# Kernel tuning notes

Hardware: AMD Instinct MI355X
Metric: run time of the kernel (lower is better)

Reference implementation:

```python
import jax, jax.numpy as jnp
import numpy as np

N_NODES = 100000
N_EDGES = 1600000
D_IN, D_H, D_OUT = 128, 128, 64


def gcn_conv(x, src, dst, W, b, n_nodes):
    """PyG GCNConv (eval): x' = D^{-1/2} (A+I) D^{-1/2} X W + b.
    src/dst already include self-loops."""
    h = x @ W  # [N, d_out] -- transform first (fewer FLOPs when d_out <= d_in)
    deg = jax.ops.segment_sum(jnp.ones_like(dst, dtype=h.dtype), dst, num_segments=n_nodes)
    dinv = jnp.where(deg > 0, jax.lax.rsqrt(deg), 0.0)
    norm = dinv[src] * dinv[dst]  # [E]
    msg = h[src] * norm[:, None]  # gather + scale
    out = jax.ops.segment_sum(msg, dst, num_segments=n_nodes)  # scatter-add
    return out + b


def setup_inputs() -> dict:
    key = jax.random.key(0)
    k = jax.random.split(key, 8)
    x = jax.random.normal(k[0], (N_NODES, D_IN), dtype=jnp.float32)
    edge_index = jax.random.randint(k[1], (2, N_EDGES), 0, N_NODES, dtype=jnp.int32)
    s = 0.1
    W1 = jax.random.normal(k[2], (D_IN, D_H), dtype=jnp.float32) * s
    b1 = jnp.zeros((D_H,), dtype=jnp.float32)
    W2 = jax.random.normal(k[3], (D_H, D_H), dtype=jnp.float32) * s
    b2 = jnp.zeros((D_H,), dtype=jnp.float32)
    W3 = jax.random.normal(k[4], (D_H, D_OUT), dtype=jnp.float32) * s
    b3 = jnp.zeros((D_OUT,), dtype=jnp.float32)
    return {"x": x, "edge_index": edge_index, "W1": W1, "b1": b1,
            "W2": W2, "b2": b2, "W3": W3, "b3": b3}


def reference(x, edge_index, W1, b1, W2, b2, W3, b3):
    n = x.shape[0]
    # add self-loops once (shared by all layers)
    loops = jnp.arange(n, dtype=edge_index.dtype)
    src = jnp.concatenate([edge_index[0], loops])
    dst = jnp.concatenate([edge_index[1], loops])
    h = gcn_conv(x, src, dst, W1, b1, n)
    h = jax.nn.relu(h)  # dropout = identity in eval mode
    h = gcn_conv(h, src, dst, W2, b2, n)
    h = jax.nn.relu(h)
    out = gcn_conv(h, src, dst, W3, b3, n)
    return out
```

## Files before the change

### kernel.cpp

```cpp
#include <hip/hip_runtime.h>
#include <hip/hip_fp16.h>

#define N_NODES 100000
#define N_EDGES 1600000
#define NBUCKET 196
#define CAP     8960
#define EPB     6250

typedef _Float16 half8 __attribute__((ext_vector_type(8)));
typedef float float4v __attribute__((ext_vector_type(4)));

__launch_bounds__(256)
__global__ void k_partition(const int* __restrict__ src, const int* __restrict__ dst,
                            int* __restrict__ bcur, int* __restrict__ ebuf, int E) {
    __shared__ int hist[200];
    __shared__ int basebkt[200];
    const int tid = threadIdx.x;
    if (tid < 200) hist[tid] = 0;
    __syncthreads();
    const int e0 = blockIdx.x * EPB, e1 = min(e0 + EPB, E);
    for (int e = e0 + tid; e < e1; e += 256) atomicAdd(&hist[dst[e] >> 9], 1);
    __syncthreads();
    if (tid < NBUCKET) {
        int h = hist[tid];
        basebkt[tid] = tid * CAP + (h ? atomicAdd(&bcur[tid], h) : 0);
    }
    __syncthreads();
    if (tid < 200) hist[tid] = 0;
    __syncthreads();
    for (int e = e0 + tid; e < e1; e += 256) {
        int d = dst[e];
        int bk = d >> 9;
        int o = atomicAdd(&hist[bk], 1);
        ebuf[basebkt[bk] + o] = (src[e] << 9) | (d & 511);
    }
}

__launch_bounds__(256)
__global__ void k_bsort(const int* __restrict__ ebuf, const int* __restrict__ bcur,
                        int* __restrict__ adj, int* __restrict__ stv,
                        int* __restrict__ deg, float* __restrict__ dinv, int N) {
    __shared__ int cnt[512];
    __shared__ int offs[512];
    const int b = blockIdx.x;
    const int tid = threadIdx.x;
    const int base = b * CAP;
    const int n_b = min(bcur[b], CAP);
    const int node0 = b << 9;
    cnt[tid] = 0; cnt[tid + 256] = 0;
    __syncthreads();
    for (int i = tid; i < n_b; i += 256)
        atomicAdd(&cnt[ebuf[base + i] & 511], 1);
    __syncthreads();
    if (tid < 64) {
        int v[8], tot = 0;
#pragma unroll
        for (int j = 0; j < 8; ++j) { int t = cnt[tid * 8 + j]; v[j] = tot; tot += t; }
        int inc = tot;
#pragma unroll
        for (int d = 1; d < 64; d <<= 1) {
            int u = __shfl_up(inc, d, 64);
            if (tid >= d) inc += u;
        }
        const int excl = inc - tot;
#pragma unroll
        for (int j = 0; j < 8; ++j) offs[tid * 8 + j] = excl + v[j];
    }
    __syncthreads();
#pragma unroll
    for (int h = 0; h < 2; ++h) {
        int local = tid + h * 256;
        int node = node0 + local;
        if (node < N) {
            stv[node] = base + offs[local];
            deg[node] = cnt[local];
            dinv[node] = rsqrtf((float)(cnt[local] + 1));
        }
    }
    __syncthreads();
    for (int i = tid; i < n_b; i += 256) {
        int pk = ebuf[base + i];
        int pos = atomicAdd(&offs[pk & 511], 1);
        adj[base + pos] = pk >> 9;
    }
}

__global__ void k_wswz_all(const float* __restrict__ W1, const float* __restrict__ W2,
                           const float* __restrict__ W3, _Float16* __restrict__ wz1,
                           _Float16* __restrict__ wz2, _Float16* __restrict__ wz3,
                           int* __restrict__ bcur) {
    if (blockIdx.x == 0) bcur[threadIdx.x] = 0;
    int t = blockIdx.x * 256 + threadIdx.x;
    const float* W; _Float16* wsz; int BN;
    if (t < 2048)      { W = W1; wsz = wz1; BN = 128; }
    else if (t < 4096) { W = W2; wsz = wz2; BN = 128; t -= 2048; }
    else if (t < 5120) { W = W3; wsz = wz3; BN = 64;  t -= 4096; }
    else return;
    const int l = t & 63;
    const int kblk = (t >> 6) & 3;
    const int nt = t >> 8;
    const int krow = kblk * 32 + ((l >> 4) << 3);
    const int col = nt * 16 + (l & 15);
    _Float16 v[8];
#pragma unroll
    for (int j = 0; j < 8; ++j) v[j] = (_Float16)W[(krow + j) * BN + col];
    *(uint4*)&wsz[t << 3] = *(uint4*)v;
}

template <int BN, bool AFP16>
__launch_bounds__(256)
__global__ void k_gemm_mfma(const void* __restrict__ Xv, const _Float16* __restrict__ wsz,
                            const float* __restrict__ dinv, __half* __restrict__ out, int N) {
    constexpr int NT = BN / 16;
    __shared__ __align__(16) _Float16 smem[BN * 128];

    const int tid = threadIdx.x;
    for (int i = tid; i < BN * 16; i += 256)
        *(uint4*)&smem[i << 3] = *(const uint4*)&wsz[i << 3];

    const int w = tid >> 6;
    const int lane = tid & 63;
    const int q = lane >> 4;
    const int m = lane & 15;
    const int row0 = blockIdx.x * 128 + w * 32;
    __syncthreads();

#pragma unroll
    for (int t = 0; t < 2; ++t) {
        const int arow = row0 + t * 16 + m;
        const int arowc = arow < N ? arow : N - 1;

        float4v acc[NT];
#pragma unroll
        for (int nt = 0; nt < NT; ++nt) acc[nt] = (float4v){0.f, 0.f, 0.f, 0.f};

#pragma unroll
        for (int kblk = 0; kblk < 4; ++kblk) {
            half8 xf;
            if constexpr (AFP16) {
                const _Float16* A = (const _Float16*)Xv + (size_t)arowc * 128 + (q << 3);
                xf = *(const half8*)(A + kblk * 32);
            } else {
                const float* A = (const float*)Xv + (size_t)arowc * 128 + (q << 3);
                float4 a0 = *(const float4*)(A + kblk * 32);
                float4 a1 = *(const float4*)(A + kblk * 32 + 4);
                xf[0] = (_Float16)a0.x; xf[1] = (_Float16)a0.y;
                xf[2] = (_Float16)a0.z; xf[3] = (_Float16)a0.w;
                xf[4] = (_Float16)a1.x; xf[5] = (_Float16)a1.y;
                xf[6] = (_Float16)a1.z; xf[7] = (_Float16)a1.w;
            }
#pragma unroll
            for (int nt = 0; nt < NT; ++nt) {
                half8 wf = *(const half8*)&smem[(((nt << 2) + kblk) << 9) + (lane << 3)];
                acc[nt] = __builtin_amdgcn_mfma_f32_16x16x32_f16(wf, xf, acc[nt], 0, 0, 0);
            }
        }

        if (arow < N) {
            const float s = dinv[arow];
#pragma unroll
            for (int nt = 0; nt < NT; ++nt) {
                _Float16 ov[4];
#pragma unroll
                for (int r = 0; r < 4; ++r) ov[r] = (_Float16)(acc[nt][r] * s);
                *(uint2*)&out[(size_t)arow * BN + nt * 16 + q * 4] = *(uint2*)ov;
            }
        }
    }
}

template <bool RELU>
__launch_bounds__(256)
__global__ void k_agg128(const __half* __restrict__ tp, const int* __restrict__ adj,
                         const int* __restrict__ startv, const int* __restrict__ deg,
                         const float* __restrict__ dinv, const float* __restrict__ bias,
                         _Float16* __restrict__ out, int N) {
    const int node = (blockIdx.x << 2) + (threadIdx.x >> 6);
    const int lane = threadIdx.x & 63;
    if (node >= N) return;
    const int s = startv[node];
    const int cnt = deg[node];
    const float di = dinv[node];
    const int g = lane >> 4;
    const int sl = lane & 15;
    const uint4* rowb = (const uint4*)tp;

    float acc[8] = {0.f, 0.f, 0.f, 0.f, 0.f, 0.f, 0.f, 0.f};
    auto addrow = [&](uint4 v) {
        float2 f0 = __half22float2(*(__half2*)&v.x);
        float2 f1 = __half22float2(*(__half2*)&v.y);
        float2 f2 = __half22float2(*(__half2*)&v.z);
        float2 f3 = __half22float2(*(__half2*)&v.w);
        acc[0] += f0.x; acc[1] += f0.y; acc[2] += f1.x; acc[3] += f1.y;
        acc[4] += f2.x; acc[5] += f2.y; acc[6] += f3.x; acc[7] += f3.y;
    };
    if (g == 0) addrow(rowb[(size_t)node * 16 + sl]);

    int e = 0;
    for (; e + 16 <= cnt; e += 16) {
        int j[4];
#pragma unroll
        for (int u = 0; u < 4; ++u) j[u] = adj[s + e + 4 * u + g];
        uint4 v[4];
#pragma unroll
        for (int u = 0; u < 4; ++u) v[u] = rowb[(size_t)j[u] * 16 + sl];
#pragma unroll
        for (int u = 0; u < 4; ++u) addrow(v[u]);
    }
    for (; e + 4 <= cnt; e += 4)
        addrow(rowb[(size_t)adj[s + e + g] * 16 + sl]);
    if (e + g < cnt)
        addrow(rowb[(size_t)adj[s + e + g] * 16 + sl]);

#pragma unroll
    for (int i = 0; i < 8; ++i) {
        acc[i] += __shfl_xor(acc[i], 32);
        acc[i] += __shfl_xor(acc[i], 16);
    }
    if (g == 0) {
        float4 b0 = *(const float4*)&bias[sl * 8];
        float4 b1 = *(const float4*)&bias[sl * 8 + 4];
        float o[8];
        o[0] = di * acc[0] + b0.x; o[1] = di * acc[1] + b0.y;
        o[2] = di * acc[2] + b0.z; o[3] = di * acc[3] + b0.w;
        o[4] = di * acc[4] + b1.x; o[5] = di * acc[5] + b1.y;
        o[6] = di * acc[6] + b1.z; o[7] = di * acc[7] + b1.w;
        if (RELU)
#pragma unroll
            for (int i = 0; i < 8; ++i) o[i] = fmaxf(o[i], 0.f);
        __half2 ov[4];
#pragma unroll
        for (int i = 0; i < 4; ++i) ov[i] = __floats2half2_rn(o[2 * i], o[2 * i + 1]);
        *(uint4*)&out[(size_t)node * 128 + sl * 8] = *(uint4*)ov;
    }
}

__launch_bounds__(256)
__global__ void k_agg64(const __half* __restrict__ tp, const int* __restrict__ adj,
                        const int* __restrict__ startv, const int* __restrict__ deg,
                        const float* __restrict__ dinv, const float* __restrict__ bias,
                        float* __restrict__ out, int N) {
    const int node = (blockIdx.x << 2) + (threadIdx.x >> 6);
    const int lane = threadIdx.x & 63;
    if (node >= N) return;
    const int s = startv[node];
    const int cnt = deg[node];
    const float di = dinv[node];
    const int g = lane >> 4;
    const int sl = lane & 15;
    const uint2* rowb = (const uint2*)tp;

    float acc[4] = {0.f, 0.f, 0.f, 0.f};
    auto addrow = [&](uint2 v) {
        float2 f0 = __half22float2(*(__half2*)&v.x);
        float2 f1 = __half22float2(*(__half2*)&v.y);
        acc[0] += f0.x; acc[1] += f0.y; acc[2] += f1.x; acc[3] += f1.y;
    };
    if (g == 0) addrow(rowb[(size_t)node * 16 + sl]);

    int e = 0;
    for (; e + 16 <= cnt; e += 16) {
        int j[4];
#pragma unroll
        for (int u = 0; u < 4; ++u) j[u] = adj[s + e + 4 * u + g];
        uint2 v[4];
#pragma unroll
        for (int u = 0; u < 4; ++u) v[u] = rowb[(size_t)j[u] * 16 + sl];
#pragma unroll
        for (int u = 0; u < 4; ++u) addrow(v[u]);
    }
    for (; e + 4 <= cnt; e += 4)
        addrow(rowb[(size_t)adj[s + e + g] * 16 + sl]);
    if (e + g < cnt)
        addrow(rowb[(size_t)adj[s + e + g] * 16 + sl]);

#pragma unroll
    for (int i = 0; i < 4; ++i) {
        acc[i] += __shfl_xor(acc[i], 32);
        acc[i] += __shfl_xor(acc[i], 16);
    }
    if (g == 0) {
        float4 bb = *(const float4*)&bias[sl * 4];
        float4 o;
        o.x = di * acc[0] + bb.x; o.y = di * acc[1] + bb.y;
        o.z = di * acc[2] + bb.z; o.w = di * acc[3] + bb.w;
        *(float4*)&out[(size_t)node * 64 + sl * 4] = o;
    }
}

extern "C" void kernel_launch(void* const* d_in, const int* in_sizes, int n_in,
                              void* d_out, int out_size, void* d_ws, size_t ws_size,
                              hipStream_t stream) {
    const float* x  = (const float*)d_in[0];
    const int*   ei = (const int*)d_in[1];
    const float* W1 = (const float*)d_in[2];
    const float* b1 = (const float*)d_in[3];
    const float* W2 = (const float*)d_in[4];
    const float* b2 = (const float*)d_in[5];
    const float* W3 = (const float*)d_in[6];
    const float* b3 = (const float*)d_in[7];
    float* out = (float*)d_out;
    const int* src = ei;
    const int* dst = ei + N_EDGES;

    char* p = (char*)d_ws;
    __half* tp      = (__half*)p;    p += (size_t)N_NODES * 128 * 2;
    _Float16* hbuf  = (_Float16*)p;  p += (size_t)N_NODES * 128 * 2;
    int*   deg  = (int*)p;    p += (size_t)N_NODES * 4;
    float* dinv = (float*)p;  p += (size_t)N_NODES * 4;
    int*   stv  = (int*)p;    p += (size_t)N_NODES * 4;
    int*   bCur = (int*)p;    p += 1024;
    int*   adj  = (int*)p;    p += (size_t)NBUCKET * CAP * 4 + 16384;
    _Float16* wz1 = (_Float16*)p; p += 16384 * 2;
    _Float16* wz2 = (_Float16*)p; p += 16384 * 2;
    _Float16* wz3 = (_Float16*)p; p += 8192 * 2;
    size_t need = (size_t)(p - (char*)d_ws);
    if (ws_size < need) return;

    int* ebuf = (int*)tp;

    k_wswz_all<<<20, 256, 0, stream>>>(W1, W2, W3, wz1, wz2, wz3, bCur);
    k_partition<<<256, 256, 0, stream>>>(src, dst, bCur, ebuf, N_EDGES);
    k_bsort<<<NBUCKET, 256, 0, stream>>>(ebuf, bCur, adj, stv, deg, dinv, N_NODES);

    const int gb = (N_NODES + 127) / 128;
    const int ab = (N_NODES + 3) / 4;
    k_gemm_mfma<128, false><<<gb, 256, 0, stream>>>(x, wz1, dinv, tp, N_NODES);
    k_agg128<true><<<ab, 256, 0, stream>>>(tp, adj, stv, deg, dinv, b1, hbuf, N_NODES);
    k_gemm_mfma<128, true><<<gb, 256, 0, stream>>>(hbuf, wz2, dinv, tp, N_NODES);
    k_agg128<true><<<ab, 256, 0, stream>>>(tp, adj, stv, deg, dinv, b2, hbuf, N_NODES);
    k_gemm_mfma<64, true><<<gb, 256, 0, stream>>>(hbuf, wz3, dinv, tp, N_NODES);
    k_agg64<<<ab, 256, 0, stream>>>(tp, adj, stv, deg, dinv, b3, out, N_NODES);
}
```

Before: 371.1 us.

## Keep GEMM weights in registers and use persistent grid-stride warps

Replaces the LDS-staged weight tile with per-lane register fragments loaded once per wave. A fixed grid of waves then loops over 16-row tiles in grid-stride fashion. All four K-slices of the A row are loaded up front before the MFMA chain. This removes repeated LDS fills and the block barrier for every 128 rows, and it allows more loads in flight. The cost is much higher register pressure (64 VGPRs of weights for BN=128), which the launch-bounds minimum-blocks hint may force into spills.

```diff
diff --git a/kernel.cpp b/kernel.cpp
--- a/kernel.cpp
+++ b/kernel.cpp
@@ -107,54 +107,55 @@
     *(uint4*)&wsz[t << 3] = *(uint4*)v;
 }
 
-template <int BN, bool AFP16>
-__launch_bounds__(256)
-__global__ void k_gemm_mfma(const void* __restrict__ Xv, const _Float16* __restrict__ wsz,
-                            const float* __restrict__ dinv, __half* __restrict__ out, int N) {
+template <int BN, bool AFP16, int MINW>
+__launch_bounds__(256, MINW)
+__global__ void k_gemm_reg(const void* __restrict__ Xv, const _Float16* __restrict__ wsz,
+                           const float* __restrict__ dinv, __half* __restrict__ out,
+                           int N, int tiles) {
     constexpr int NT = BN / 16;
-    __shared__ __align__(16) _Float16 smem[BN * 128];
-
-    const int tid = threadIdx.x;
-    for (int i = tid; i < BN * 16; i += 256)
-        *(uint4*)&smem[i << 3] = *(const uint4*)&wsz[i << 3];
-
-    const int w = tid >> 6;
-    const int lane = tid & 63;
+    const int lane = threadIdx.x & 63;
     const int q = lane >> 4;
     const int m = lane & 15;
-    const int row0 = blockIdx.x * 128 + w * 32;
-    __syncthreads();
-
-#pragma unroll
-    for (int t = 0; t < 2; ++t) {
-        const int arow = row0 + t * 16 + m;
+
+    half8 wreg[NT * 4];
+#pragma unroll
+    for (int f = 0; f < NT * 4; ++f)
+        wreg[f] = *(const half8*)&wsz[(f << 9) + (lane << 3)];
+
+    const int wid = (blockIdx.x * 256 + threadIdx.x) >> 6;
+    const int nw = gridDim.x * 4;
+
+    for (int tile = wid; tile < tiles; tile += nw) {
+        const int arow = tile * 16 + m;
         const int arowc = arow < N ? arow : N - 1;
 
-        float4v acc[NT];
-#pragma unroll
-        for (int nt = 0; nt < NT; ++nt) acc[nt] = (float4v){0.f, 0.f, 0.f, 0.f};
-
-#pragma unroll
-        for (int kblk = 0; kblk < 4; ++kblk) {
-            half8 xf;
-            if constexpr (AFP16) {
-                const _Float16* A = (const _Float16*)Xv + (size_t)arowc * 128 + (q << 3);
-                xf = *(const half8*)(A + kblk * 32);
-            } else {
-                const float* A = (const float*)Xv + (size_t)arowc * 128 + (q << 3);
-                float4 a0 = *(const float4*)(A + kblk * 32);
-                float4 a1 = *(const float4*)(A + kblk * 32 + 4);
-                xf[0] = (_Float16)a0.x; xf[1] = (_Float16)a0.y;
-                xf[2] = (_Float16)a0.z; xf[3] = (_Float16)a0.w;
-                xf[4] = (_Float16)a1.x; xf[5] = (_Float16)a1.y;
-                xf[6] = (_Float16)a1.z; xf[7] = (_Float16)a1.w;
-            }
-#pragma unroll
-            for (int nt = 0; nt < NT; ++nt) {
-                half8 wf = *(const half8*)&smem[(((nt << 2) + kblk) << 9) + (lane << 3)];
-                acc[nt] = __builtin_amdgcn_mfma_f32_16x16x32_f16(wf, xf, acc[nt], 0, 0, 0);
+        half8 xf[4];
+        if constexpr (AFP16) {
+            const _Float16* A = (const _Float16*)Xv + (size_t)arowc * 128 + (q << 3);
+#pragma unroll
+            for (int kb = 0; kb < 4; ++kb) xf[kb] = *(const half8*)(A + kb * 32);
+        } else {
+            const float* A = (const float*)Xv + (size_t)arowc * 128 + (q << 3);
+#pragma unroll
+            for (int kb = 0; kb < 4; ++kb) {
+                float4 a0 = *(const float4*)(A + kb * 32);
+                float4 a1 = *(const float4*)(A + kb * 32 + 4);
+                xf[kb][0] = (_Float16)a0.x; xf[kb][1] = (_Float16)a0.y;
+                xf[kb][2] = (_Float16)a0.z; xf[kb][3] = (_Float16)a0.w;
+                xf[kb][4] = (_Float16)a1.x; xf[kb][5] = (_Float16)a1.y;
+                xf[kb][6] = (_Float16)a1.z; xf[kb][7] = (_Float16)a1.w;
             }
         }
+
+        float4v acc[NT];
+#pragma unroll
+        for (int nt = 0; nt < NT; ++nt) acc[nt] = (float4v){0.f, 0.f, 0.f, 0.f};
+#pragma unroll
+        for (int kb = 0; kb < 4; ++kb)
+#pragma unroll
+            for (int nt = 0; nt < NT; ++nt)
+                acc[nt] = __builtin_amdgcn_mfma_f32_16x16x32_f16(wreg[nt * 4 + kb], xf[kb],
+                                                                acc[nt], 0, 0, 0);
 
         if (arow < N) {
             const float s = dinv[arow];
@@ -323,12 +324,12 @@
     k_partition<<<256, 256, 0, stream>>>(src, dst, bCur, ebuf, N_EDGES);
     k_bsort<<<NBUCKET, 256, 0, stream>>>(ebuf, bCur, adj, stv, deg, dinv, N_NODES);
 
-    const int gb = (N_NODES + 127) / 128;
+    const int tiles = (N_NODES + 15) / 16;
     const int ab = (N_NODES + 3) / 4;
-    k_gemm_mfma<128, false><<<gb, 256, 0, stream>>>(x, wz1, dinv, tp, N_NODES);
+    k_gemm_reg<128, false, 2><<<512, 256, 0, stream>>>(x, wz1, dinv, tp, N_NODES, tiles);
     k_agg128<true><<<ab, 256, 0, stream>>>(tp, adj, stv, deg, dinv, b1, hbuf, N_NODES);
-    k_gemm_mfma<128, true><<<gb, 256, 0, stream>>>(hbuf, wz2, dinv, tp, N_NODES);
+    k_gemm_reg<128, true, 2><<<512, 256, 0, stream>>>(hbuf, wz2, dinv, tp, N_NODES, tiles);
     k_agg128<true><<<ab, 256, 0, stream>>>(tp, adj, stv, deg, dinv, b2, hbuf, N_NODES);
-    k_gemm_mfma<64, true><<<gb, 256, 0, stream>>>(hbuf, wz3, dinv, tp, N_NODES);
+    k_gemm_reg<64, true, 4><<<1024, 256, 0, stream>>>(hbuf, wz3, dinv, tp, N_NODES, tiles);
     k_agg64<<<ab, 256, 0, stream>>>(tp, adj, stv, deg, dinv, b3, out, N_NODES);
 }
```

Result: no change. 367.9 us (-0.9%).
